# Performance work log

Hardware: AMD Instinct MI355X
Metric: run time of the kernel (lower is better)

The kernel has to match this reference:

```python
import jax, jax.numpy as jnp
import numpy as np

INF = 1000000000000.0
HEAD_SIZE = 64
HEADS = 12
MAX_LENGTH = 512


def _rope_tables(dim, max_length):
    inv_freq = 1.0 / (10000.0 ** (jnp.arange(0, dim, 2, dtype=jnp.float32) / dim))
    t = jnp.arange(max_length, dtype=jnp.float32)
    freqs = t[:, None] * inv_freq[None, :]  # [L, dim/2]
    return jnp.sin(freqs), jnp.cos(freqs)


def _apply_rope(t, sin, cos):
    # t: [B, L, d]; sin/cos: [L, d/2]
    t1, t2 = t[..., 0::2], t[..., 1::2]
    out = jnp.stack([t1 * cos - t2 * sin, t1 * sin + t2 * cos], axis=-1)
    return out.reshape(t.shape)


def setup_inputs() -> dict:
    key = jax.random.key(0)
    k1, k2, k3, k4, k5 = jax.random.split(key, 5)
    B, L, H = 16, 512, 1024
    inputs = jax.random.normal(k1, (B, L, H), dtype=jnp.float32)
    attention_mask = jnp.ones((B, L), dtype=jnp.float32)
    s1 = 1.0 / np.sqrt(H)
    s2 = 1.0 / np.sqrt(HEAD_SIZE * 2)
    W1 = jax.random.normal(k2, (H, HEAD_SIZE * 2), dtype=jnp.float32) * s1
    b1 = jax.random.normal(k3, (HEAD_SIZE * 2,), dtype=jnp.float32) * s1
    W2 = jax.random.normal(k4, (HEAD_SIZE * 2, HEADS * 2), dtype=jnp.float32) * s2
    b2 = jax.random.normal(k5, (HEADS * 2,), dtype=jnp.float32) * s2
    return {"inputs": inputs, "attention_mask": attention_mask,
            "W1": W1, "b1": b1, "W2": W2, "b2": b2}


def reference(inputs, attention_mask, W1, b1, W2, b2):
    B, L, _ = inputs.shape
    x = inputs @ W1 + b1                      # [B, L, 2*head_size]
    qw, kw = x[..., 0::2], x[..., 1::2]        # [B, L, head_size] each
    sin, cos = _rope_tables(HEAD_SIZE, MAX_LENGTH)
    sin, cos = sin[:L], cos[:L]
    qw = _apply_rope(qw, sin, cos)
    kw = _apply_rope(kw, sin, cos)
    logits = jnp.einsum('bmd,bnd->bmn', qw, kw) / (HEAD_SIZE ** 0.5)  # [B, L, L]
    bias = jnp.swapaxes(x @ W2 + b2, 1, 2) / 2.0                       # [B, 2*heads, L]
    # logits[b,h,m,n] = score[b,m,n] + bias_even[b,h,n] + bias_odd[b,h,m]
    logits = logits[:, None] + bias[:, 0::2, None, :] + bias[:, 1::2, :, None]
    attn_mask = 1.0 - attention_mask[:, None, None, :] * attention_mask[:, None, :, None]
    logits = logits - attn_mask * INF
    tril = jnp.tril(jnp.ones((L, L), dtype=logits.dtype), k=-1)
    logits = logits - tril * INF
    return logits
```

## Files before the change

kernel.cpp:

```cpp
#include <hip/hip_runtime.h>
#include <hip/hip_bf16.h>

typedef short bf16x8 __attribute__((ext_vector_type(8)));
typedef float f32x4 __attribute__((ext_vector_type(4)));
typedef unsigned short u16;
typedef unsigned short u16x8 __attribute__((ext_vector_type(8)));

#define FINF 1.0e12f

__device__ __forceinline__ u16 f2b(float f) {
  union { float f; unsigned int u; } x; x.f = f;
  unsigned int r = x.u + 0x7fffu + ((x.u >> 16) & 1u);
  return (u16)(r >> 16);
}

__global__ __launch_bounds__(256) void k0_w1frag(const float* __restrict__ W1,
                                                 u16* __restrict__ w1f) {
  int idx = blockIdx.x * 256 + threadIdx.x;
  int k = idx >> 7, c = idx & 127;
  float v = W1[idx];
  int chunk = k >> 6, kk = k & 63;
  int ks = kk >> 5, km = kk & 31, kg = km >> 3, i = km & 7;
  int nt = c >> 4, ln = c & 15;
  int dst = chunk * 8192 + (nt * 2 + ks) * 512 + (kg * 16 + ln) * 8 + i;
  w1f[dst] = f2b(v);
}

__global__ __launch_bounds__(256) void k1_prep(
    const float* __restrict__ inputs, const u16* __restrict__ w1f,
    const float* __restrict__ b1, const float* __restrict__ W2,
    const float* __restrict__ b2,
    u16* __restrict__ qw, u16* __restrict__ kw,
    float* __restrict__ biasE, float* __restrict__ biasO) {
  __shared__ __align__(16) char smem[53632];
  float* w2t = (float*)(smem + 40960);
  float* xt  = (float*)smem;

  int t = threadIdx.x;
  int lane = t & 63, w = t >> 6;
  int r0 = blockIdx.x * 32;
  int b = r0 >> 9, l0 = r0 & 511;

  #pragma unroll
  for (int i = 0; i < 12; ++i) {
    int idx = t + i * 256;
    int k = idx / 24, c = idx - k * 24;
    w2t[c * 132 + k] = W2[idx];
  }

  f32x4 acc[4];
  #pragma unroll
  for (int nti = 0; nti < 4; ++nti) acc[nti] = (f32x4){0.f, 0.f, 0.f, 0.f};

  int wr = (w & 1) * 16;
  int wnt = (w >> 1) * 4;

  int arow_s = t >> 3;
  const float* ain = &inputs[(size_t)(r0 + arow_s) * 1024 + (t & 7) * 8];
  int abyt = (arow_s * 128 + (t & 7) * 16) ^ ((arow_s & 7) << 4);
  const float4* wsrcAll = (const float4*)w1f;

  float4 a0 = *(const float4*)(ain);
  float4 a1 = *(const float4*)(ain + 4);
  float4 wr0 = wsrcAll[t];
  float4 wr1 = wsrcAll[t + 256];
  float4 wr2 = wsrcAll[t + 512];
  float4 wr3 = wsrcAll[t + 768];
  {
    u16x8 av;
    av[0] = f2b(a0.x); av[1] = f2b(a0.y); av[2] = f2b(a0.z); av[3] = f2b(a0.w);
    av[4] = f2b(a1.x); av[5] = f2b(a1.y); av[6] = f2b(a1.z); av[7] = f2b(a1.w);
    *(u16x8*)(smem + abyt) = av;
    float4* wd = (float4*)(smem + 8192);
    wd[t] = wr0; wd[t + 256] = wr1; wd[t + 512] = wr2; wd[t + 768] = wr3;
  }
  __syncthreads();

  for (int ch = 0; ch < 16; ++ch) {
    if (ch < 15) {
      a0 = *(const float4*)(ain + (ch + 1) * 64);
      a1 = *(const float4*)(ain + (ch + 1) * 64 + 4);
      const float4* wsrc = wsrcAll + (ch + 1) * 1024;
      wr0 = wsrc[t]; wr1 = wsrc[t + 256]; wr2 = wsrc[t + 512]; wr3 = wsrc[t + 768];
    }
    {
      const char* Ab = smem + (ch & 1) * 4096;
      const u16* Wb = (const u16*)(smem + 8192 + (ch & 1) * 16384);
      int arow = wr + (lane & 15);
      int hi = lane >> 4;
      #pragma unroll
      for (int ks = 0; ks < 2; ++ks) {
        int cb = ks * 64 + hi * 16;
        bf16x8 a = *(const bf16x8*)(Ab + ((arow * 128 + cb) ^ ((arow & 7) << 4)));
        #pragma unroll
        for (int nti = 0; nti < 4; ++nti) {
          int nt = wnt + nti;
          bf16x8 bb = *(const bf16x8*)&Wb[((nt * 2 + ks) * 64 + lane) * 8];
          acc[nti] = __builtin_amdgcn_mfma_f32_16x16x32_bf16(a, bb, acc[nti], 0, 0, 0);
        }
      }
    }
    if (ch < 15) {
      int q = (ch + 1) & 1;
      u16x8 av;
      av[0] = f2b(a0.x); av[1] = f2b(a0.y); av[2] = f2b(a0.z); av[3] = f2b(a0.w);
      av[4] = f2b(a1.x); av[5] = f2b(a1.y); av[6] = f2b(a1.z); av[7] = f2b(a1.w);
      *(u16x8*)(smem + q * 4096 + abyt) = av;
      float4* wd = (float4*)(smem + 8192 + q * 16384);
      wd[t] = wr0; wd[t + 256] = wr1; wd[t + 512] = wr2; wd[t + 768] = wr3;
    }
    __syncthreads();
  }
  __syncthreads();

  #pragma unroll
  for (int nti = 0; nti < 4; ++nti) {
    int c = (wnt + nti) * 16 + (lane & 15);
    float b1v = b1[c];
    #pragma unroll
    for (int r = 0; r < 4; ++r) {
      int row = wr + ((lane >> 4) << 2) + r;
      xt[row * 132 + c] = acc[nti][r] + b1v;
    }
  }
  __syncthreads();

  {
    int r = t >> 3, jb = (t & 7) * 4;
    int l = l0 + r;
    float fl = (float)l;
    u16x8 qv, kv;
    #pragma unroll
    for (int p = 0; p < 4; ++p) {
      int j = jb + p;
      float4 x4 = *(const float4*)&xt[r * 132 + 4 * j];
      float invf = exp2f(-0.4152410118609203f * (float)j);
      float ang = fl * invf;
      float rev = ang * 0.15915494309189535f;
      rev = rev - floorf(rev);
      float sv, cv;
      __sincosf(rev * 6.2831853071795864f, &sv, &cv);
      qv[2 * p] = f2b(x4.x * cv - x4.z * sv);
      qv[2 * p + 1] = f2b(x4.x * sv + x4.z * cv);
      kv[2 * p] = f2b(x4.y * cv - x4.w * sv);
      kv[2 * p + 1] = f2b(x4.y * sv + x4.w * cv);
    }
    size_t base = ((size_t)(b * 512 + l)) * 64 + jb * 2;
    *(u16x8*)&qw[base] = qv;
    *(u16x8*)&kw[base] = kv;
  }

  if (t < 192) {
    int c = t >> 3;
    int rg = (t & 7) * 4;
    float s0 = b2[c], s1 = s0, s2 = s0, s3 = s0;
    #pragma unroll
    for (int k4 = 0; k4 < 32; ++k4) {
      float4 wv = *(const float4*)&w2t[c * 132 + k4 * 4];
      float4 x0 = *(const float4*)&xt[(rg + 0) * 132 + k4 * 4];
      float4 x1 = *(const float4*)&xt[(rg + 1) * 132 + k4 * 4];
      float4 x2 = *(const float4*)&xt[(rg + 2) * 132 + k4 * 4];
      float4 x3 = *(const float4*)&xt[(rg + 3) * 132 + k4 * 4];
      s0 += x0.x * wv.x + x0.y * wv.y + x0.z * wv.z + x0.w * wv.w;
      s1 += x1.x * wv.x + x1.y * wv.y + x1.z * wv.z + x1.w * wv.w;
      s2 += x2.x * wv.x + x2.y * wv.y + x2.z * wv.z + x2.w * wv.w;
      s3 += x3.x * wv.x + x3.y * wv.y + x3.z * wv.z + x3.w * wv.w;
    }
    int h = c >> 1;
    size_t o = ((size_t)(b * 12 + h)) * 512 + l0 + rg;
    float4 sv = {s0 * 0.5f, s1 * 0.5f, s2 * 0.5f, s3 * 0.5f};
    if (c & 1) *(float4*)&biasO[o] = sv;
    else       *(float4*)&biasE[o] = sv;
  }
}

__global__ __launch_bounds__(256) void k2_main(
    const u16* __restrict__ qw, const u16* __restrict__ kw,
    const float* __restrict__ biasE, const float* __restrict__ biasO,
    const float* __restrict__ amask, float* __restrict__ out) {
  __shared__ char smem[24448];
  u16* Q = (u16*)smem;
  u16* K = (u16*)(smem + 8192);
  float* qkL = (float*)smem;
  float* BN = (float*)(smem + 17408);
  float* BM = (float*)(smem + 17408 + 3264);
  float* AMm = (float*)(smem + 17408 + 6528);
  float* AMn = AMm + 64;

  int t = threadIdx.x;
  int lane = t & 63, w = t >> 6;
  int n0 = blockIdx.x * 64, m0 = blockIdx.y * 64, b = blockIdx.z;
  bool skip = (m0 >= n0 + 64);

  if (!skip) {
    int row = t >> 2, sg = t & 3;
    const u16x8* qsrc = (const u16x8*)&qw[((size_t)(b * 512 + m0 + row)) * 64 + sg * 16];
    u16x8 q0 = qsrc[0], q1 = qsrc[1];
    const u16x8* ksrc = (const u16x8*)&kw[((size_t)(b * 512 + n0 + row)) * 64 + sg * 16];
    u16x8 k0v = ksrc[0], k1v = ksrc[1];
    int swz = (row & 7) << 4;
    int byt = row * 128 + sg * 32;
    *(u16x8*)((char*)Q + ((byt) ^ swz)) = q0;
    *(u16x8*)((char*)Q + ((byt + 16) ^ swz)) = q1;
    *(u16x8*)((char*)K + ((byt) ^ swz)) = k0v;
    *(u16x8*)((char*)K + ((byt + 16) ^ swz)) = k1v;
  }
  if (t < 192) {
    int h = t >> 4, kq = t & 15;
    *(float4*)&BN[h * 68 + kq * 4] =
        *(const float4*)&biasE[((size_t)(b * 12 + h)) * 512 + n0 + kq * 4];
    *(float4*)&BM[h * 68 + kq * 4] =
        *(const float4*)&biasO[((size_t)(b * 12 + h)) * 512 + m0 + kq * 4];
  } else if (t < 224) {
    int i = t - 192;
    if (i < 16) *(float4*)&AMm[i * 4] = *(const float4*)&amask[b * 512 + m0 + i * 4];
    else { int ii = i - 16; *(float4*)&AMn[ii * 4] = *(const float4*)&amask[b * 512 + n0 + ii * 4]; }
  }
  __syncthreads();

  if (!skip) {
    f32x4 acc[4];
    #pragma unroll
    for (int nt = 0; nt < 4; ++nt) acc[nt] = (f32x4){0.f, 0.f, 0.f, 0.f};
    int mrow = w * 16 + (lane & 15);
    int hi = lane >> 4;
    #pragma unroll
    for (int ks = 0; ks < 2; ++ks) {
      int cb = ks * 64 + hi * 16;
      bf16x8 a = *(const bf16x8*)((const char*)Q +
                                  ((mrow * 128 + cb) ^ ((mrow & 7) << 4)));
      #pragma unroll
      for (int nt = 0; nt < 4; ++nt) {
        int nr = nt * 16 + (lane & 15);
        bf16x8 bb = *(const bf16x8*)((const char*)K +
                                     ((nr * 128 + cb) ^ ((nr & 7) << 4)));
        acc[nt] = __builtin_amdgcn_mfma_f32_16x16x32_bf16(a, bb, acc[nt], 0, 0, 0);
      }
    }
    __syncthreads();
    #pragma unroll
    for (int nt = 0; nt < 4; ++nt)
      #pragma unroll
      for (int r = 0; r < 4; ++r)
        qkL[(w * 16 + hi * 4 + r) * 68 + nt * 16 + (lane & 15)] = acc[nt][r];
    __syncthreads();
  }

  int a15 = t & 15, mb = t >> 4;
  float amn0 = AMn[a15 * 4 + 0], amn1 = AMn[a15 * 4 + 1];
  float amn2 = AMn[a15 * 4 + 2], amn3 = AMn[a15 * 4 + 3];
  float vals[4][4];
  #pragma unroll
  for (int mi = 0; mi < 4; ++mi) {
    int m = mb + 16 * mi;
    int mg = m0 + m;
    float amm = AMm[m];
    int ng = n0 + a15 * 4;
    float p0 = (1.f - amm * amn0) * FINF + ((mg > ng + 0) ? FINF : 0.f);
    float p1 = (1.f - amm * amn1) * FINF + ((mg > ng + 1) ? FINF : 0.f);
    float p2 = (1.f - amm * amn2) * FINF + ((mg > ng + 2) ? FINF : 0.f);
    float p3 = (1.f - amm * amn3) * FINF + ((mg > ng + 3) ? FINF : 0.f);
    if (!skip) {
      float4 qk = *(const float4*)&qkL[m * 68 + a15 * 4];
      vals[mi][0] = qk.x * 0.125f - p0;
      vals[mi][1] = qk.y * 0.125f - p1;
      vals[mi][2] = qk.z * 0.125f - p2;
      vals[mi][3] = qk.w * 0.125f - p3;
    } else {
      vals[mi][0] = -p0; vals[mi][1] = -p1; vals[mi][2] = -p2; vals[mi][3] = -p3;
    }
  }

  size_t outbase = (size_t)(b * 12) * 262144 + (size_t)m0 * 512 + n0 + a15 * 4;
  #pragma unroll
  for (int h = 0; h < 12; ++h) {
    float4 bn = *(const float4*)&BN[h * 68 + a15 * 4];
    #pragma unroll
    for (int mi = 0; mi < 4; ++mi) {
      int m = mb + 16 * mi;
      float bm = BM[h * 68 + m];
      float4 v;
      v.x = vals[mi][0] + bn.x + bm;
      v.y = vals[mi][1] + bn.y + bm;
      v.z = vals[mi][2] + bn.z + bm;
      v.w = vals[mi][3] + bn.w + bm;
      *(float4*)&out[outbase + (size_t)h * 262144 + (size_t)m * 512] = v;
    }
  }
}

extern "C" void kernel_launch(void* const* d_in, const int* in_sizes, int n_in,
                              void* d_out, int out_size, void* d_ws, size_t ws_size,
                              hipStream_t stream) {
  const float* inputs = (const float*)d_in[0];
  const float* amask  = (const float*)d_in[1];
  const float* W1     = (const float*)d_in[2];
  const float* b1     = (const float*)d_in[3];
  const float* W2     = (const float*)d_in[4];
  const float* b2     = (const float*)d_in[5];
  float* out = (float*)d_out;

  char* ws = (char*)d_ws;
  u16* qw      = (u16*)(ws);
  u16* kw      = (u16*)(ws + (1u << 20));
  float* biasE = (float*)(ws + (2u << 20));
  float* biasO = (float*)(ws + (2u << 20) + 393216u);
  u16* w1f     = (u16*)(ws + (2u << 20) + 786432u);

  k0_w1frag<<<512, 256, 0, stream>>>(W1, w1f);
  k1_prep<<<256, 256, 0, stream>>>(inputs, w1f, b1, W2, b2, qw, kw, biasE, biasO);
  k2_main<<<dim3(8, 8, 16), 256, 0, stream>>>(qw, kw, biasE, biasO, amask, out);
}
```

Baseline: 57.44 us.

## Retile main kernel to 32x256 blocks for full-row contiguous output stores

Changes the k2_main tile from 64x64 to 32 rows by 256 columns. Each wave now writes 1KB-contiguous row segments per head, and the K tile, bias and mask loads are reorganised to fit. The goal is more coalesced, longer write bursts for the large output, which is write-bandwidth bound, and fewer blocks. In exchange it uses more LDS (about 51KB), which may lower occupancy, and fewer tiles can skip the QK matmul below the diagonal.

```diff
diff --git a/kernel.cpp b/kernel.cpp
--- a/kernel.cpp
+++ b/kernel.cpp
@@ -178,112 +178,115 @@
     const u16* __restrict__ qw, const u16* __restrict__ kw,
     const float* __restrict__ biasE, const float* __restrict__ biasO,
     const float* __restrict__ amask, float* __restrict__ out) {
-  __shared__ char smem[24448];
-  u16* Q = (u16*)smem;
-  u16* K = (u16*)(smem + 8192);
+  __shared__ __align__(16) char smem[52224];
   float* qkL = (float*)smem;
-  float* BN = (float*)(smem + 17408);
-  float* BM = (float*)(smem + 17408 + 3264);
-  float* AMm = (float*)(smem + 17408 + 6528);
-  float* AMn = AMm + 64;
+  float* BN  = (float*)(smem + 36864);
+  float* BM  = (float*)(smem + 49344);
+  float* AMm = (float*)(smem + 51072);
+  float* AMn = (float*)(smem + 51200);
 
   int t = threadIdx.x;
   int lane = t & 63, w = t >> 6;
-  int n0 = blockIdx.x * 64, m0 = blockIdx.y * 64, b = blockIdx.z;
-  bool skip = (m0 >= n0 + 64);
+  int n0 = blockIdx.x * 256, m0 = blockIdx.y * 32, b = blockIdx.z;
+  bool skip = (m0 >= n0 + 256);
 
   if (!skip) {
-    int row = t >> 2, sg = t & 3;
-    const u16x8* qsrc = (const u16x8*)&qw[((size_t)(b * 512 + m0 + row)) * 64 + sg * 16];
-    u16x8 q0 = qsrc[0], q1 = qsrc[1];
-    const u16x8* ksrc = (const u16x8*)&kw[((size_t)(b * 512 + n0 + row)) * 64 + sg * 16];
-    u16x8 k0v = ksrc[0], k1v = ksrc[1];
-    int swz = (row & 7) << 4;
-    int byt = row * 128 + sg * 32;
-    *(u16x8*)((char*)Q + ((byt) ^ swz)) = q0;
-    *(u16x8*)((char*)Q + ((byt + 16) ^ swz)) = q1;
-    *(u16x8*)((char*)K + ((byt) ^ swz)) = k0v;
-    *(u16x8*)((char*)K + ((byt + 16) ^ swz)) = k1v;
-  }
-  if (t < 192) {
-    int h = t >> 4, kq = t & 15;
-    *(float4*)&BN[h * 68 + kq * 4] =
-        *(const float4*)&biasE[((size_t)(b * 12 + h)) * 512 + n0 + kq * 4];
-    *(float4*)&BM[h * 68 + kq * 4] =
-        *(const float4*)&biasO[((size_t)(b * 12 + h)) * 512 + m0 + kq * 4];
-  } else if (t < 224) {
-    int i = t - 192;
-    if (i < 16) *(float4*)&AMm[i * 4] = *(const float4*)&amask[b * 512 + m0 + i * 4];
-    else { int ii = i - 16; *(float4*)&AMn[ii * 4] = *(const float4*)&amask[b * 512 + n0 + ii * 4]; }
+    int qrow = t >> 3, qseg = t & 7;
+    u16x8 qv = *(const u16x8*)&qw[((size_t)(b * 512 + m0 + qrow)) * 64 + qseg * 8];
+    *(u16x8*)(smem + ((qrow * 128 + qseg * 16) ^ ((qrow & 7) << 4))) = qv;
+    #pragma unroll
+    for (int rep = 0; rep < 8; ++rep) {
+      int idx = t + rep * 256;
+      int krow = idx >> 3, kseg = idx & 7;
+      u16x8 kv = *(const u16x8*)&kw[((size_t)(b * 512 + n0 + krow)) * 64 + kseg * 8];
+      *(u16x8*)(smem + 4096 + ((krow * 128 + kseg * 16) ^ ((krow & 7) << 4))) = kv;
+    }
+  }
+  #pragma unroll
+  for (int rep = 0; rep < 3; ++rep) {
+    int idx = t + rep * 256;
+    int h = idx >> 6, col = (idx & 63) * 4;
+    *(float4*)&BN[h * 260 + col] =
+        *(const float4*)&biasE[((size_t)(b * 12 + h)) * 512 + n0 + col];
+  }
+  if (t < 96) {
+    int h = t >> 3, col = (t & 7) * 4;
+    *(float4*)&BM[h * 36 + col] =
+        *(const float4*)&biasO[((size_t)(b * 12 + h)) * 512 + m0 + col];
+  } else if (t < 104) {
+    int i = t - 96;
+    *(float4*)&AMm[i * 4] = *(const float4*)&amask[b * 512 + m0 + i * 4];
+  } else if (t < 168) {
+    int i = t - 104;
+    *(float4*)&AMn[i * 4] = *(const float4*)&amask[b * 512 + n0 + i * 4];
   }
   __syncthreads();
 
   if (!skip) {
-    f32x4 acc[4];
-    #pragma unroll
-    for (int nt = 0; nt < 4; ++nt) acc[nt] = (f32x4){0.f, 0.f, 0.f, 0.f};
-    int mrow = w * 16 + (lane & 15);
+    f32x4 acc[8];
+    #pragma unroll
+    for (int nt = 0; nt < 8; ++nt) acc[nt] = (f32x4){0.f, 0.f, 0.f, 0.f};
+    int mh = w & 1, nh = w >> 1;
+    int mrow = mh * 16 + (lane & 15);
     int hi = lane >> 4;
     #pragma unroll
     for (int ks = 0; ks < 2; ++ks) {
       int cb = ks * 64 + hi * 16;
-      bf16x8 a = *(const bf16x8*)((const char*)Q +
-                                  ((mrow * 128 + cb) ^ ((mrow & 7) << 4)));
+      bf16x8 a = *(const bf16x8*)(smem + ((mrow * 128 + cb) ^ ((mrow & 7) << 4)));
       #pragma unroll
-      for (int nt = 0; nt < 4; ++nt) {
-        int nr = nt * 16 + (lane & 15);
-        bf16x8 bb = *(const bf16x8*)((const char*)K +
+      for (int nt = 0; nt < 8; ++nt) {
+        int nr = nh * 128 + nt * 16 + (lane & 15);
+        bf16x8 bb = *(const bf16x8*)(smem + 4096 +
                                      ((nr * 128 + cb) ^ ((nr & 7) << 4)));
         acc[nt] = __builtin_amdgcn_mfma_f32_16x16x32_bf16(a, bb, acc[nt], 0, 0, 0);
       }
     }
     __syncthreads();
     #pragma unroll
-    for (int nt = 0; nt < 4; ++nt)
+    for (int nt = 0; nt < 8; ++nt)
       #pragma unroll
       for (int r = 0; r < 4; ++r)
-        qkL[(w * 16 + hi * 4 + r) * 68 + nt * 16 + (lane & 15)] = acc[nt][r];
+        qkL[(mh * 16 + hi * 4 + r) * 260 + nh * 128 + nt * 16 + (lane & 15)] =
+            acc[nt][r];
     __syncthreads();
   }
 
-  int a15 = t & 15, mb = t >> 4;
-  float amn0 = AMn[a15 * 4 + 0], amn1 = AMn[a15 * 4 + 1];
-  float amn2 = AMn[a15 * 4 + 2], amn3 = AMn[a15 * 4 + 3];
-  float vals[4][4];
-  #pragma unroll
-  for (int mi = 0; mi < 4; ++mi) {
-    int m = mb + 16 * mi;
+  float4 amn = *(const float4*)&AMn[lane * 4];
+  float vals[8][4];
+  #pragma unroll
+  for (int i = 0; i < 8; ++i) {
+    int m = w * 8 + i;
     int mg = m0 + m;
     float amm = AMm[m];
-    int ng = n0 + a15 * 4;
-    float p0 = (1.f - amm * amn0) * FINF + ((mg > ng + 0) ? FINF : 0.f);
-    float p1 = (1.f - amm * amn1) * FINF + ((mg > ng + 1) ? FINF : 0.f);
-    float p2 = (1.f - amm * amn2) * FINF + ((mg > ng + 2) ? FINF : 0.f);
-    float p3 = (1.f - amm * amn3) * FINF + ((mg > ng + 3) ? FINF : 0.f);
+    int ng = n0 + lane * 4;
+    float p0 = (1.f - amm * amn.x) * FINF + ((mg > ng + 0) ? FINF : 0.f);
+    float p1 = (1.f - amm * amn.y) * FINF + ((mg > ng + 1) ? FINF : 0.f);
+    float p2 = (1.f - amm * amn.z) * FINF + ((mg > ng + 2) ? FINF : 0.f);
+    float p3 = (1.f - amm * amn.w) * FINF + ((mg > ng + 3) ? FINF : 0.f);
     if (!skip) {
-      float4 qk = *(const float4*)&qkL[m * 68 + a15 * 4];
-      vals[mi][0] = qk.x * 0.125f - p0;
-      vals[mi][1] = qk.y * 0.125f - p1;
-      vals[mi][2] = qk.z * 0.125f - p2;
-      vals[mi][3] = qk.w * 0.125f - p3;
+      float4 qk = *(const float4*)&qkL[m * 260 + lane * 4];
+      vals[i][0] = qk.x * 0.125f - p0;
+      vals[i][1] = qk.y * 0.125f - p1;
+      vals[i][2] = qk.z * 0.125f - p2;
+      vals[i][3] = qk.w * 0.125f - p3;
     } else {
-      vals[mi][0] = -p0; vals[mi][1] = -p1; vals[mi][2] = -p2; vals[mi][3] = -p3;
-    }
-  }
-
-  size_t outbase = (size_t)(b * 12) * 262144 + (size_t)m0 * 512 + n0 + a15 * 4;
+      vals[i][0] = -p0; vals[i][1] = -p1; vals[i][2] = -p2; vals[i][3] = -p3;
+    }
+  }
+
+  size_t outbase = (size_t)(b * 12) * 262144 + (size_t)m0 * 512 + n0 + lane * 4;
   #pragma unroll
   for (int h = 0; h < 12; ++h) {
-    float4 bn = *(const float4*)&BN[h * 68 + a15 * 4];
-    #pragma unroll
-    for (int mi = 0; mi < 4; ++mi) {
-      int m = mb + 16 * mi;
-      float bm = BM[h * 68 + m];
+    float4 bn = *(const float4*)&BN[h * 260 + lane * 4];
+    #pragma unroll
+    for (int i = 0; i < 8; ++i) {
+      int m = w * 8 + i;
+      float bm = BM[h * 36 + m];
       float4 v;
-      v.x = vals[mi][0] + bn.x + bm;
-      v.y = vals[mi][1] + bn.y + bm;
-      v.z = vals[mi][2] + bn.z + bm;
-      v.w = vals[mi][3] + bn.w + bm;
+      v.x = vals[i][0] + bn.x + bm;
+      v.y = vals[i][1] + bn.y + bm;
+      v.z = vals[i][2] + bn.z + bm;
+      v.w = vals[i][3] + bn.w + bm;
       *(float4*)&out[outbase + (size_t)h * 262144 + (size_t)m * 512] = v;
     }
   }
@@ -309,5 +312,5 @@
 
   k0_w1frag<<<512, 256, 0, stream>>>(W1, w1f);
   k1_prep<<<256, 256, 0, stream>>>(inputs, w1f, b1, W2, b2, qw, kw, biasE, biasO);
-  k2_main<<<dim3(8, 8, 16), 256, 0, stream>>>(qw, kw, biasE, biasO, amask, out);
-}
+  k2_main<<<dim3(2, 16, 16), 256, 0, stream>>>(qw, kw, biasE, biasO, amask, out);
+}
```

After: 58.21 us. Within noise of the previous version (+1.3%).
